# Kernel optimization log

Measured on AMD Instinct MI355X. Metric: run time of the kernel, lower is better.

## Reference

```python
import jax, jax.numpy as jnp
import numpy as np

D_K = 64
D_MODEL = 1024
N_HEADS = 16


def setup_inputs() -> dict:
    key = jax.random.key(0)
    ks = jax.random.split(key, 9)
    B, S = 2, 2048
    scale = 1.0 / np.sqrt(D_MODEL)
    inp = {
        "x": jax.random.normal(ks[0], (B, S, D_MODEL), dtype=jnp.float32),
        "w_q": jax.random.normal(ks[1], (D_MODEL, N_HEADS * D_K), dtype=jnp.float32) * scale,
        "b_q": jnp.zeros((N_HEADS * D_K,), dtype=jnp.float32),
        "w_k": jax.random.normal(ks[2], (D_MODEL, N_HEADS * D_K), dtype=jnp.float32) * scale,
        "b_k": jnp.zeros((N_HEADS * D_K,), dtype=jnp.float32),
        "w_v": jax.random.normal(ks[3], (D_MODEL, N_HEADS * D_K), dtype=jnp.float32) * scale,
        "b_v": jnp.zeros((N_HEADS * D_K,), dtype=jnp.float32),
        "w_o": jax.random.normal(ks[4], (N_HEADS * D_K, D_MODEL), dtype=jnp.float32) * scale,
        "b_o": jnp.zeros((D_MODEL,), dtype=jnp.float32),
    }
    return inp


def reference(x, w_q, b_q, w_k, b_k, w_v, b_v, w_o, b_o):
    B, S, _ = x.shape
    H, Dk = N_HEADS, D_K

    def split_heads(m):  # [B,S,H*Dk] -> [B,H,S,Dk]
        return m.reshape(B, S, H, Dk).transpose(0, 2, 1, 3)

    Q = split_heads(x @ w_q + b_q)
    K = split_heads(x @ w_k + b_k)
    V = split_heads(x @ w_v + b_v)

    scores = jnp.einsum("bhsd,bhtd->bhst", Q, K) / jnp.sqrt(jnp.float32(Dk))
    probs = jax.nn.softmax(scores, axis=-1)
    attn = jnp.einsum("bhst,bhtd->bhsd", probs, V)  # [B,H,S,Dk]
    attn = attn.transpose(0, 2, 1, 3).reshape(B, S, H * Dk)
    return attn @ w_o + b_o
```

## Files before the change

kernel.cpp:

```cpp
#include <hip/hip_runtime.h>
#include <math.h>

#define D_MODELc 1024
#define N_HEADSc 16
#define D_Kc     64
#define B_SZc    2
#define S_LENc   2048
#define NTOKc    (B_SZc * S_LENc)

using half8  = __attribute__((ext_vector_type(8))) _Float16;
using half4  = __attribute__((ext_vector_type(4))) _Float16;
using fp16x2 = __attribute__((ext_vector_type(2))) __fp16;
using float4v = __attribute__((ext_vector_type(4))) float;

__global__ __launch_bounds__(256) void cvt_all(
    const float* __restrict__ x,
    const float* __restrict__ W0, const float* __restrict__ W1,
    const float* __restrict__ W2, const float* __restrict__ W3,
    _Float16* __restrict__ wout, _Float16* __restrict__ xout)
{
    __shared__ float T[32][33];
    const int z = blockIdx.z;
    const int t = threadIdx.x;

    if (z == 4) {
        const int bid = blockIdx.y * 32 + blockIdx.x;
        #pragma unroll
        for (int c = 0; c < 2; ++c) {
            const int i = bid * 512 + c * 256 + t;
            float4v a = ((const float4v*)x)[2 * i];
            float4v b = ((const float4v*)x)[2 * i + 1];
            half8 h;
            h[0] = (_Float16)a[0]; h[1] = (_Float16)a[1];
            h[2] = (_Float16)a[2]; h[3] = (_Float16)a[3];
            h[4] = (_Float16)b[0]; h[5] = (_Float16)b[1];
            h[6] = (_Float16)b[2]; h[7] = (_Float16)b[3];
            ((half8*)xout)[i] = h;
        }
        return;
    }

    const float* W = (z == 0) ? W0 : (z == 1) ? W1 : (z == 2) ? W2 : W3;
    _Float16* O = wout + (size_t)z * 1024 * 1024;

    const int k0 = blockIdx.x * 32;
    const int n0 = blockIdx.y * 32;
    {
        const int r = t >> 3, c4 = (t & 7) * 4;
        float4v v = *(const float4v*)(W + (size_t)(k0 + r) * 1024 + n0 + c4);
        T[r][c4 + 0] = v[0]; T[r][c4 + 1] = v[1];
        T[r][c4 + 2] = v[2]; T[r][c4 + 3] = v[3];
    }
    __syncthreads();
    {
        const int rn = t >> 3, ck4 = (t & 7) * 4;
        half4 h;
        h[0] = (_Float16)T[ck4 + 0][rn];
        h[1] = (_Float16)T[ck4 + 1][rn];
        h[2] = (_Float16)T[ck4 + 2][rn];
        h[3] = (_Float16)T[ck4 + 3][rn];
        *(half4*)(O + (size_t)(n0 + rn) * 1024 + k0 + ck4) = h;
    }
}

__global__ __launch_bounds__(256) void gemm_qkv(
    const _Float16* __restrict__ A, const _Float16* __restrict__ BtAll,
    const float* __restrict__ bias0, const float* __restrict__ bias1,
    const float* __restrict__ bias2, _Float16* __restrict__ Cout)
{
    __shared__ _Float16 Als[2][128 * 32];
    __shared__ _Float16 Bls[2][128 * 32];

    constexpr int K = 1024;
    const int tid = threadIdx.x;

    const int flat = blockIdx.x + 32 * blockIdx.y + 256 * blockIdx.z;
    const int xcd  = flat & 7;
    const int slot = flat >> 3;
    const int m0   = ((xcd & 3) * 8 + (slot & 7)) * 128;
    const int n0   = ((xcd >> 2) * 4 + ((slot >> 3) & 3)) * 128;
    const int z    = slot >> 5;

    const _Float16* Bt  = BtAll + (size_t)z * 1024 * 1024;
    const float* bias   = (z == 0) ? bias0 : (z == 1) ? bias1 : bias2;
    const float qscale  = (z == 0) ? 0.18033688011112042f : 1.0f;

    const int wave = tid >> 6, lane = tid & 63;
    const int wr = wave >> 1, wc = wave & 1;
    const int quad = lane >> 4, l16 = lane & 15;

    float4v acc[4][4];
    #pragma unroll
    for (int i = 0; i < 4; ++i)
        #pragma unroll
        for (int j = 0; j < 4; ++j)
            acc[i][j] = (float4v){0.f, 0.f, 0.f, 0.f};

    for (int k0 = 0; k0 < K; k0 += 64) {
        #pragma unroll
        for (int c = 0; c < 2; ++c) {
            const int i   = c * 256 + tid;
            const int row = i >> 2, kc = i & 3;
            #pragma unroll
            for (int h = 0; h < 2; ++h) {
                __builtin_amdgcn_global_load_lds(
                    (const __attribute__((address_space(1))) void*)
                        (A + (size_t)(m0 + row) * K + k0 + h * 32 + kc * 8),
                    (__attribute__((address_space(3))) void*)(Als[h] + i * 8),
                    16, 0, 0);
                __builtin_amdgcn_global_load_lds(
                    (const __attribute__((address_space(1))) void*)
                        (Bt + (size_t)(n0 + row) * K + k0 + h * 32 + kc * 8),
                    (__attribute__((address_space(3))) void*)(Bls[h] + i * 8),
                    16, 0, 0);
            }
        }
        __syncthreads();

        half8 af[4][2], bf[4][2];
        #pragma unroll
        for (int i = 0; i < 4; ++i) {
            const int r = (wr * 64 + i * 16 + l16) * 32 + quad * 8;
            af[i][0] = *(const half8*)(Als[0] + r);
            af[i][1] = *(const half8*)(Als[1] + r);
        }
        #pragma unroll
        for (int j = 0; j < 4; ++j) {
            const int r = (wc * 64 + j * 16 + l16) * 32 + quad * 8;
            bf[j][0] = *(const half8*)(Bls[0] + r);
            bf[j][1] = *(const half8*)(Bls[1] + r);
        }
        #pragma unroll
        for (int i = 0; i < 4; ++i)
            #pragma unroll
            for (int j = 0; j < 4; ++j) {
                acc[i][j] = __builtin_amdgcn_mfma_f32_16x16x32_f16(
                    af[i][0], bf[j][0], acc[i][j], 0, 0, 0);
                acc[i][j] = __builtin_amdgcn_mfma_f32_16x16x32_f16(
                    af[i][1], bf[j][1], acc[i][j], 0, 0, 0);
            }
        __syncthreads();
    }

    if (z != 2) {
        _Float16* C = Cout + (size_t)z * NTOKc * D_MODELc;
        #pragma unroll
        for (int i = 0; i < 4; ++i) {
            const int rbase = m0 + wr * 64 + i * 16 + quad * 4;
            #pragma unroll
            for (int j = 0; j < 4; ++j) {
                const int col = n0 + wc * 64 + j * 16 + l16;
                const float bv = bias[col];
                #pragma unroll
                for (int r = 0; r < 4; ++r)
                    C[(size_t)(rbase + r) * 1024 + col] =
                        (_Float16)((acc[i][j][r] + bv) * qscale);
            }
        }
    } else {
        #pragma unroll
        for (int i = 0; i < 4; ++i) {
            const int rbase = m0 + wr * 64 + i * 16 + quad * 4;
            const int b = rbase >> 11, s0 = rbase & 2047;
            #pragma unroll
            for (int j = 0; j < 4; ++j) {
                const int col = n0 + wc * 64 + j * 16 + l16;
                const float bv = bias[col];
                const int h = col >> 6, d = col & 63;
                half4 hv;
                #pragma unroll
                for (int r = 0; r < 4; ++r)
                    hv[r] = (_Float16)(acc[i][j][r] + bv);
                _Float16* C = Cout + (size_t)2 * NTOKc * D_MODELc;
                *(half4*)(C + (((size_t)(b * N_HEADSc + h)) * D_Kc + d) *
                          S_LENc + s0) = hv;
            }
        }
    }
}

__global__ __launch_bounds__(256) void gemm_out(
    const _Float16* __restrict__ A, const _Float16* __restrict__ Bt,
    const float* __restrict__ bias, float* __restrict__ C)
{
    __shared__ _Float16 Als[2][64 * 32];
    __shared__ _Float16 Bls[2][128 * 32];

    constexpr int K = 1024;
    const int tid = threadIdx.x;
    const int m0  = blockIdx.x * 64;
    const int n0  = blockIdx.y * 128;

    const int wave = tid >> 6, lane = tid & 63;
    const int wr = wave >> 1, wc = wave & 1;
    const int quad = lane >> 4, l16 = lane & 15;

    float4v acc[2][4];
    #pragma unroll
    for (int i = 0; i < 2; ++i)
        #pragma unroll
        for (int j = 0; j < 4; ++j)
            acc[i][j] = (float4v){0.f, 0.f, 0.f, 0.f};

    for (int k0 = 0; k0 < K; k0 += 64) {
        {
            const int row = tid >> 2, kc = tid & 3;
            #pragma unroll
            for (int h = 0; h < 2; ++h)
                __builtin_amdgcn_global_load_lds(
                    (const __attribute__((address_space(1))) void*)
                        (A + (size_t)(m0 + row) * K + k0 + h * 32 + kc * 8),
                    (__attribute__((address_space(3))) void*)(Als[h] + tid * 8),
                    16, 0, 0);
        }
        #pragma unroll
        for (int c = 0; c < 2; ++c) {
            const int i = c * 256 + tid;
            const int row = i >> 2, kc = i & 3;
            #pragma unroll
            for (int h = 0; h < 2; ++h)
                __builtin_amdgcn_global_load_lds(
                    (const __attribute__((address_space(1))) void*)
                        (Bt + (size_t)(n0 + row) * K + k0 + h * 32 + kc * 8),
                    (__attribute__((address_space(3))) void*)(Bls[h] + i * 8),
                    16, 0, 0);
        }
        __syncthreads();

        half8 af[2][2], bf[4][2];
        #pragma unroll
        for (int i = 0; i < 2; ++i) {
            const int r = (wr * 32 + i * 16 + l16) * 32 + quad * 8;
            af[i][0] = *(const half8*)(Als[0] + r);
            af[i][1] = *(const half8*)(Als[1] + r);
        }
        #pragma unroll
        for (int j = 0; j < 4; ++j) {
            const int r = (wc * 64 + j * 16 + l16) * 32 + quad * 8;
            bf[j][0] = *(const half8*)(Bls[0] + r);
            bf[j][1] = *(const half8*)(Bls[1] + r);
        }
        #pragma unroll
        for (int i = 0; i < 2; ++i)
            #pragma unroll
            for (int j = 0; j < 4; ++j) {
                acc[i][j] = __builtin_amdgcn_mfma_f32_16x16x32_f16(
                    af[i][0], bf[j][0], acc[i][j], 0, 0, 0);
                acc[i][j] = __builtin_amdgcn_mfma_f32_16x16x32_f16(
                    af[i][1], bf[j][1], acc[i][j], 0, 0, 0);
            }
        __syncthreads();
    }

    #pragma unroll
    for (int i = 0; i < 2; ++i) {
        const int rbase = m0 + wr * 32 + i * 16 + quad * 4;
        #pragma unroll
        for (int j = 0; j < 4; ++j) {
            const int col = n0 + wc * 64 + j * 16 + l16;
            const float bv = bias[col];
            #pragma unroll
            for (int r = 0; r < 4; ++r)
                C[(size_t)(rbase + r) * 1024 + col] = acc[i][j][r] + bv;
        }
    }
}

__global__ __launch_bounds__(256) void attn_mfma(
    const _Float16* __restrict__ Qt, const _Float16* __restrict__ Kt,
    const _Float16* __restrict__ Vtg, _Float16* __restrict__ Ab)
{
    __shared__ _Float16 Ks[2][64 * 64];
    __shared__ _Float16 Vt[64 * 64];
    __shared__ _Float16 Ps[64 * 64];
    __shared__ float Lsh[64];

    const int tid  = threadIdx.x;
    const int wv   = tid >> 6;
    const int lane = tid & 63;
    const int quad = lane >> 4;
    const int l16  = lane & 15;
    const int rotl = (l16 & 7) << 3;
    const int cA   = (quad * 8 + rotl) & 63;
    const int cB   = (quad * 8 + 32 + rotl) & 63;

    const int flat = blockIdx.x + 32 * blockIdx.y;
    const int slot = flat >> 3;
    const int bh   = (flat & 7) + 8 * (slot >> 5);
    const int q0   = (slot & 31) * 64;
    const int b  = bh >> 4, h = bh & 15;

    const _Float16* Qsl = Qt + (size_t)b * S_LENc * D_MODELc + h * 64;
    const _Float16* Ksl = Kt + (size_t)b * S_LENc * D_MODELc + h * 64;
    const _Float16* Vsl = Vtg + (size_t)bh * S_LENc * D_Kc;

    const int sR = tid >> 3;
    const int sC = (((tid & 7) - ((tid >> 3) & 7)) & 7) << 3;
    const _Float16* gK = Ksl + (size_t)sR * D_MODELc + sC;
    const _Float16* gV = Vsl + (size_t)sR * S_LENc + sC;

#define STAGE_K(BUF, T0)                                                     \
    {                                                                        \
        _Pragma("unroll")                                                    \
        for (int c = 0; c < 2; ++c)                                          \
            __builtin_amdgcn_global_load_lds(                                \
                (const __attribute__((address_space(1))) void*)              \
                    (gK + (size_t)((T0) + c * 32) * D_MODELc),               \
                (__attribute__((address_space(3))) void*)                    \
                    (Ks[BUF] + tid * 8 + c * 2048),                          \
                16, 0, 0);                                                   \
    }
#define STAGE_V(T0)                                                          \
    {                                                                        \
        _Pragma("unroll")                                                    \
        for (int c = 0; c < 2; ++c)                                          \
            __builtin_amdgcn_global_load_lds(                                \
                (const __attribute__((address_space(1))) void*)              \
                    (gV + (T0) + c * 32 * S_LENc),                           \
                (__attribute__((address_space(3))) void*)                    \
                    (Vt + tid * 8 + c * 2048),                               \
                16, 0, 0);                                                   \
    }

    half8 aq[4][2];
    #pragma unroll
    for (int qf = 0; qf < 4; ++qf) {
        const _Float16* qp = Qsl + (size_t)(q0 + qf * 16 + l16) * D_MODELc;
        aq[qf][0] = *(const half8*)(qp + quad * 8);
        aq[qf][1] = *(const half8*)(qp + 32 + quad * 8);
    }

    half8 vones;
    #pragma unroll
    for (int j = 0; j < 8; ++j) vones[j] = (_Float16)1.0f;

    float4v O[4];
    #pragma unroll
    for (int qf = 0; qf < 4; ++qf)
        O[qf] = (float4v){0.f, 0.f, 0.f, 0.f};
    float4v Lacc = (float4v){0.f, 0.f, 0.f, 0.f};

    STAGE_K(0, 0);
    STAGE_V(0);

    int cur = 0;
    for (int t0 = 0; t0 < S_LENc; t0 += 64) {
        __syncthreads();
        if (t0 != 0)
            STAGE_V(t0);

        const _Float16* KsC = Ks[cur];
        const int kbase = (wv * 16 + l16) * 64;
        half8 kf0 = *(const half8*)(KsC + kbase + cA);
        half8 kf1 = *(const half8*)(KsC + kbase + cB);

        __builtin_amdgcn_s_setprio(1);
        float4v st[4];
        #pragma unroll
        for (int qf = 0; qf < 4; ++qf) {
            st[qf] = __builtin_amdgcn_mfma_f32_16x16x32_f16(
                kf0, aq[qf][0], (float4v){0.f, 0.f, 0.f, 0.f}, 0, 0, 0);
            st[qf] = __builtin_amdgcn_mfma_f32_16x16x32_f16(
                kf1, aq[qf][1], st[qf], 0, 0, 0);
        }
        __builtin_amdgcn_s_setprio(0);

        #pragma unroll
        for (int qf = 0; qf < 4; ++qf) {
            const float p0 = __builtin_amdgcn_exp2f(fminf(st[qf][0], 15.5f));
            const float p1 = __builtin_amdgcn_exp2f(fminf(st[qf][1], 15.5f));
            const float p2 = __builtin_amdgcn_exp2f(fminf(st[qf][2], 15.5f));
            const float p3 = __builtin_amdgcn_exp2f(fminf(st[qf][3], 15.5f));
            union { fp16x2 h2[2]; half4 h4; } u;
            u.h2[0] = __builtin_amdgcn_cvt_pkrtz(p0, p1);
            u.h2[1] = __builtin_amdgcn_cvt_pkrtz(p2, p3);
            *(half4*)(Ps + (qf * 16 + l16) * 64 +
                      ((wv * 16 + quad * 4 + rotl) & 63)) = u.h4;
        }

        __syncthreads();
        if (t0 + 64 < S_LENc)
            STAGE_K(cur ^ 1, t0 + 64);

        const int vbase = (wv * 16 + l16) * 64;
        half8 bv0 = *(const half8*)(Vt + vbase + cA);
        half8 bv1 = *(const half8*)(Vt + vbase + cB);

        __builtin_amdgcn_s_setprio(1);
        #pragma unroll
        for (int qf = 0; qf < 4; ++qf) {
            const int rowP = (qf * 16 + l16) * 64;
            half8 ap0 = *(const half8*)(Ps + rowP + cA);
            half8 ap1 = *(const half8*)(Ps + rowP + cB);
            O[qf] = __builtin_amdgcn_mfma_f32_16x16x32_f16(
                ap0, bv0, O[qf], 0, 0, 0);
            O[qf] = __builtin_amdgcn_mfma_f32_16x16x32_f16(
                ap1, bv1, O[qf], 0, 0, 0);
            if (qf == wv) {
                Lacc = __builtin_amdgcn_mfma_f32_16x16x32_f16(
                    ap0, vones, Lacc, 0, 0, 0);
                Lacc = __builtin_amdgcn_mfma_f32_16x16x32_f16(
                    ap1, vones, Lacc, 0, 0, 0);
            }
        }
        __builtin_amdgcn_s_setprio(0);
        cur ^= 1;
    }
#undef STAGE_K
#undef STAGE_V

    if (l16 == 0) {
        #pragma unroll
        for (int r = 0; r < 4; ++r)
            Lsh[wv * 16 + quad * 4 + r] = Lacc[r];
    }
    __syncthreads();
    _Float16* Asl = Ab + (size_t)b * S_LENc * D_MODELc + h * 64;
    #pragma unroll
    for (int qf = 0; qf < 4; ++qf) {
        #pragma unroll
        for (int r = 0; r < 4; ++r) {
            const int qr = qf * 16 + quad * 4 + r;
            const float inv = 1.0f / Lsh[qr];
            Asl[(size_t)(q0 + qr) * D_MODELc + wv * 16 + l16] =
                (_Float16)(O[qf][r] * inv);
        }
    }
}

extern "C" void kernel_launch(void* const* d_in, const int* in_sizes, int n_in,
                              void* d_out, int out_size, void* d_ws, size_t ws_size,
                              hipStream_t stream)
{
    const float* x  = (const float*)d_in[0];
    const float* wq = (const float*)d_in[1];
    const float* bq = (const float*)d_in[2];
    const float* wk = (const float*)d_in[3];
    const float* bk = (const float*)d_in[4];
    const float* wv = (const float*)d_in[5];
    const float* bv = (const float*)d_in[6];
    const float* wo = (const float*)d_in[7];
    const float* bo = (const float*)d_in[8];
    float* out = (float*)d_out;

    const size_t M1 = 1024 * 1024;
    const size_t M4 = 4 * M1;
    _Float16* xh = (_Float16*)d_ws;
    _Float16* wh = xh + M4;
    _Float16* Qh = wh + M4;
    _Float16* Ah = xh;

    cvt_all<<<dim3(32, 32, 5), dim3(256), 0, stream>>>(
        x, wq, wk, wv, wo, wh, xh);
    gemm_qkv<<<dim3(NTOKc / 128, D_MODELc / 128, 3), dim3(256), 0, stream>>>(
        xh, wh, bq, bk, bv, Qh);
    attn_mfma<<<dim3(S_LENc / 64, B_SZc * N_HEADSc), dim3(256), 0, stream>>>(
        Qh, Qh + M4, Qh + 2 * M4, Ah);
    gemm_out<<<dim3(NTOKc / 64, D_MODELc / 128), dim3(256), 0, stream>>>(
        Ah, wh + 3 * M1, bo, out);
}
```

Measured before the change: 202.7 us.

## Double-buffer the QKV projection GEMM k-loop with async LDS prefetch

The QKV projection GEMM previously loaded a 64-wide k-slab into LDS, synchronized, computed, then synchronized again before the next load. It now uses two 32-wide LDS buffers: it prefetches the next slab with global_load_lds while running MFMAs on the current one, with a single barrier per step. This aims to hide global-load latency behind matrix math. In exchange, each barrier covers half the MFMA work, and correctness relies on the barrier draining the outstanding async loads.

```diff
diff --git a/kernel.cpp b/kernel.cpp
--- a/kernel.cpp
+++ b/kernel.cpp
@@ -89,6 +89,25 @@
     const int wr = wave >> 1, wc = wave & 1;
     const int quad = lane >> 4, l16 = lane & 15;
 
+#define STAGE(BUF, KS)                                                       \
+    {                                                                        \
+        _Pragma("unroll")                                                    \
+        for (int c = 0; c < 2; ++c) {                                        \
+            const int i   = c * 256 + tid;                                   \
+            const int row = i >> 2, kc = i & 3;                              \
+            __builtin_amdgcn_global_load_lds(                                \
+                (const __attribute__((address_space(1))) void*)              \
+                    (A + (size_t)(m0 + row) * K + (KS) + kc * 8),            \
+                (__attribute__((address_space(3))) void*)(Als[BUF] + i * 8), \
+                16, 0, 0);                                                   \
+            __builtin_amdgcn_global_load_lds(                                \
+                (const __attribute__((address_space(1))) void*)              \
+                    (Bt + (size_t)(n0 + row) * K + (KS) + kc * 8),           \
+                (__attribute__((address_space(3))) void*)(Bls[BUF] + i * 8), \
+                16, 0, 0);                                                   \
+        }                                                                    \
+    }
+
     float4v acc[4][4];
     #pragma unroll
     for (int i = 0; i < 4; ++i)
@@ -96,51 +115,31 @@
         for (int j = 0; j < 4; ++j)
             acc[i][j] = (float4v){0.f, 0.f, 0.f, 0.f};
 
-    for (int k0 = 0; k0 < K; k0 += 64) {
-        #pragma unroll
-        for (int c = 0; c < 2; ++c) {
-            const int i   = c * 256 + tid;
-            const int row = i >> 2, kc = i & 3;
-            #pragma unroll
-            for (int h = 0; h < 2; ++h) {
-                __builtin_amdgcn_global_load_lds(
-                    (const __attribute__((address_space(1))) void*)
-                        (A + (size_t)(m0 + row) * K + k0 + h * 32 + kc * 8),
-                    (__attribute__((address_space(3))) void*)(Als[h] + i * 8),
-                    16, 0, 0);
-                __builtin_amdgcn_global_load_lds(
-                    (const __attribute__((address_space(1))) void*)
-                        (Bt + (size_t)(n0 + row) * K + k0 + h * 32 + kc * 8),
-                    (__attribute__((address_space(3))) void*)(Bls[h] + i * 8),
-                    16, 0, 0);
-            }
-        }
+    STAGE(0, 0);
+    int cur = 0;
+    for (int ks = 0; ks < K; ks += 32) {
         __syncthreads();
-
-        half8 af[4][2], bf[4][2];
-        #pragma unroll
-        for (int i = 0; i < 4; ++i) {
-            const int r = (wr * 64 + i * 16 + l16) * 32 + quad * 8;
-            af[i][0] = *(const half8*)(Als[0] + r);
-            af[i][1] = *(const half8*)(Als[1] + r);
-        }
-        #pragma unroll
-        for (int j = 0; j < 4; ++j) {
-            const int r = (wc * 64 + j * 16 + l16) * 32 + quad * 8;
-            bf[j][0] = *(const half8*)(Bls[0] + r);
-            bf[j][1] = *(const half8*)(Bls[1] + r);
-        }
+        if (ks + 32 < K)
+            STAGE(cur ^ 1, ks + 32);
+
+        half8 af[4], bf[4];
         #pragma unroll
         for (int i = 0; i < 4; ++i)
-            #pragma unroll
-            for (int j = 0; j < 4; ++j) {
+            af[i] = *(const half8*)(Als[cur] +
+                     (wr * 64 + i * 16 + l16) * 32 + quad * 8);
+        #pragma unroll
+        for (int j = 0; j < 4; ++j)
+            bf[j] = *(const half8*)(Bls[cur] +
+                     (wc * 64 + j * 16 + l16) * 32 + quad * 8);
+        #pragma unroll
+        for (int i = 0; i < 4; ++i)
+            #pragma unroll
+            for (int j = 0; j < 4; ++j)
                 acc[i][j] = __builtin_amdgcn_mfma_f32_16x16x32_f16(
-                    af[i][0], bf[j][0], acc[i][j], 0, 0, 0);
-                acc[i][j] = __builtin_amdgcn_mfma_f32_16x16x32_f16(
-                    af[i][1], bf[j][1], acc[i][j], 0, 0, 0);
-            }
-        __syncthreads();
-    }
+                    af[i], bf[j], acc[i][j], 0, 0, 0);
+        cur ^= 1;
+    }
+#undef STAGE
 
     if (z != 2) {
         _Float16* C = Cout + (size_t)z * NTOKc * D_MODELc;
```

Result: slower. 214.0 us (+5.6%).
